# Performance work log

Hardware: AMD Instinct MI355X
Metric: run time of the kernel (lower is better)

Reference implementation:

```python
import jax, jax.numpy as jnp
import numpy as np

B, C, D = 4, 512, 1024
N = 8           # num_experts
DFF = 4096      # GEGLU inner dim; in-projection outputs 2*DFF


def setup_inputs() -> dict:
    key = jax.random.key(0)
    ks = jax.random.split(key, 7)
    hidden_states = jax.random.normal(ks[0], (B, C, D), dtype=jnp.float32)
    # Dispatch mask: one-hot expert assignment per token (top-1 routing).
    assign = jax.random.randint(ks[1], (B, C), 0, N)
    dispatch_mask = jax.nn.one_hot(assign, N, dtype=jnp.float32)        # [B,C,N]
    # Combine mask: same sparsity pattern, scaled by a router probability.
    probs = jax.random.uniform(ks[2], (B, C, 1), dtype=jnp.float32)
    combine_mask = dispatch_mask * probs                                 # [B,C,N]
    s_in = 1.0 / np.sqrt(D)
    s_out = 1.0 / np.sqrt(DFF)
    W_in = jax.random.normal(ks[3], (N, 2 * DFF, D), dtype=jnp.float32) * s_in
    b_in = jax.random.normal(ks[4], (N, 2 * DFF), dtype=jnp.float32) * 0.01
    W_out = jax.random.normal(ks[5], (N, D, DFF), dtype=jnp.float32) * s_out
    b_out = jax.random.normal(ks[6], (N, D), dtype=jnp.float32) * 0.01
    return {"hidden_states": hidden_states, "dispatch_mask": dispatch_mask,
            "combine_mask": combine_mask, "W_in": W_in, "b_in": b_in,
            "W_out": W_out, "b_out": b_out}


def reference(hidden_states, dispatch_mask, combine_mask, W_in, b_in, W_out, b_out):
    # Dispatch: [B,C,D] x [B,C,N] -> [N,B,C,D]
    h = jnp.einsum('bcd,bcn->nbcd', hidden_states, dispatch_mask)
    # Per-expert GEGLU FFN.
    h = jnp.einsum('nbcd,nfd->nbcf', h, W_in) + b_in[:, None, None, :]   # [N,B,C,2*DFF]
    x, gate = jnp.split(h, 2, axis=-1)
    h = x * jax.nn.gelu(gate, approximate=False)                          # torch F.gelu = exact erf
    h = jnp.einsum('nbcd,nfd->nbcf', h, W_out) + b_out[:, None, None, :]  # [N,B,C,D]
    # Combine: [N,B,C,D] x [B,C,N] -> [B,C,D]
    return jnp.einsum('nbcd,bcn->bcd', h, combine_mask)
```

## Files before the change

kernel.cpp:

```cpp
#include <hip/hip_runtime.h>
#include <math.h>

#define NTOK 2048
#define DDIM 1024
#define NEXP 8
#define DFF 4096
#define TWODFF 8192

typedef __attribute__((ext_vector_type(8))) short bf16x8;
typedef __attribute__((ext_vector_type(4))) float f32x4;

__device__ __forceinline__ short f2bf(float f) {
  unsigned u = __builtin_bit_cast(unsigned, f);
  u = (u + 0x7FFFu + ((u >> 16) & 1u)) >> 16;
  return (short)u;
}

__device__ __forceinline__ unsigned pk2(float a, float b) {
  unsigned r;
  asm("v_cvt_pk_bf16_f32 %0, %1, %2" : "=v"(r) : "v"(a), "v"(b));
  return r;
}

__device__ __forceinline__ void ldsbar() {
  asm volatile("s_waitcnt lgkmcnt(0)" ::: "memory");
  __builtin_amdgcn_s_barrier();
}

__global__ void route_k(const float* __restrict__ disp, const float* __restrict__ comb,
                        int* __restrict__ cnt, int* __restrict__ tokl,
                        float* __restrict__ scale) {
  __shared__ int lcnt[NEXP];
  const int tid = threadIdx.x;
  if (tid < NEXP) lcnt[tid] = 0;
  __syncthreads();
  for (int i = 0; i < 8; ++i) {
    const int t = i * 256 + tid;
    const float* row = disp + (size_t)t * NEXP;
    int e = 0;
#pragma unroll
    for (int n = 1; n < NEXP; ++n) e = (row[n] > row[e]) ? n : e;
    const float p = comb[(size_t)t * NEXP + e];
    const int slot = atomicAdd(&lcnt[e], 1);
    tokl[e * NTOK + slot] = t;
    scale[t] = p;
  }
  __syncthreads();
  if (tid < NEXP) cnt[tid] = lcnt[tid];
}

#define G1_LOAD(sa, sb, k0) do {                                              \
  _Pragma("unroll") for (int i_ = 0; i_ < 4; ++i_) {                          \
    sb[i_] = *(const float4*)(bP[i_] + (k0));                                 \
    sa[i_] = aP[i_] ? *(const float4*)(aP[i_] + (k0))                         \
                    : make_float4(0.f, 0.f, 0.f, 0.f);                        \
  } } while (0)

#define G1_STORE(sa, sb, buf) do {                                            \
  _Pragma("unroll") for (int i_ = 0; i_ < 4; ++i_) {                          \
    const int row_ = i_ * 32 + r0;                                            \
    const int off_ = row_ * 80 + (tid & 7) * 8;                               \
    uint2 va_, vb_;                                                           \
    va_.x = pk2(sa[i_].x, sa[i_].y); va_.y = pk2(sa[i_].z, sa[i_].w);         \
    vb_.x = pk2(sb[i_].x, sb[i_].y); vb_.y = pk2(sb[i_].z, sb[i_].w);         \
    *(uint2*)(Al[buf] + off_) = va_;                                          \
    *(uint2*)(Bl[buf] + off_) = vb_;                                          \
  } } while (0)

__global__ __launch_bounds__(256) void gemm1_k(
    const float* __restrict__ hid, const float* __restrict__ Win,
    const float* __restrict__ bin, const int* __restrict__ cnt,
    const int* __restrict__ tokl, short* __restrict__ act) {
  const int e = blockIdx.z;
  const int Me = cnt[e];
  const int m0 = blockIdx.y * 128;
  if (m0 >= Me) return;
  const int f0 = blockIdx.x * 64;

  __shared__ char Al[2][128 * 80];
  __shared__ char Bl[2][128 * 80];
  __shared__ int tokids[128];

  const int tid = threadIdx.x;
  if (tid < 128) {
    const int r = m0 + tid;
    tokids[tid] = (r < Me) ? tokl[e * NTOK + r] : -1;
  }
  __syncthreads();

  const int r0 = tid >> 3;
  const int c0 = (tid & 7) * 4;
  const float* aP[4];
  const float* bP[4];
#pragma unroll
  for (int i = 0; i < 4; ++i) {
    const int row = i * 32 + r0;
    const int tk = tokids[row];
    aP[i] = (tk >= 0) ? (hid + (size_t)tk * DDIM + c0) : nullptr;
    const int wr = (row < 64) ? (f0 + row) : (DFF + f0 + (row - 64));
    bP[i] = Win + (size_t)e * TWODFF * DDIM + (size_t)wr * DDIM + c0;
  }

  const int wid = tid >> 6, lane = tid & 63;
  const int wm = (wid >> 1) * 64;
  const int wf = (wid & 1) * 32;
  const int lr = lane & 15;
  const int kc = (lane >> 4) * 16;

  f32x4 accx[4][2], accg[4][2];
  const f32x4 zf = {0.f, 0.f, 0.f, 0.f};
#pragma unroll
  for (int a = 0; a < 4; ++a)
#pragma unroll
    for (int b = 0; b < 2; ++b) { accx[a][b] = zf; accg[a][b] = zf; }

  float4 sAa[4], sBa[4], sAb[4], sBb[4];
  G1_LOAD(sAa, sBa, 0);
  G1_STORE(sAa, sBa, 0);
  G1_LOAD(sAb, sBb, 32);
  ldsbar();

  for (int kt = 0; kt < 32; ++kt) {
    if (kt < 30) {
      if (kt & 1) G1_LOAD(sAb, sBb, (kt + 2) * 32);
      else        G1_LOAD(sAa, sBa, (kt + 2) * 32);
    }
    const char* Ab = Al[kt & 1];
    const char* Bb = Bl[kt & 1];
    bf16x8 a[4], bx[2], bg[2];
#pragma unroll
    for (int fm = 0; fm < 4; ++fm) {
      const int row = wm + fm * 16 + lr;
      a[fm] = *(const bf16x8*)(Ab + row * 80 + kc);
    }
#pragma unroll
    for (int ff = 0; ff < 2; ++ff) {
      const int rx = wf + ff * 16 + lr;
      bx[ff] = *(const bf16x8*)(Bb + rx * 80 + kc);
      bg[ff] = *(const bf16x8*)(Bb + (rx + 64) * 80 + kc);
    }
#pragma unroll
    for (int fm = 0; fm < 4; ++fm)
#pragma unroll
      for (int ff = 0; ff < 2; ++ff) {
        accx[fm][ff] = __builtin_amdgcn_mfma_f32_16x16x32_bf16(a[fm], bx[ff], accx[fm][ff], 0, 0, 0);
        accg[fm][ff] = __builtin_amdgcn_mfma_f32_16x16x32_bf16(a[fm], bg[ff], accg[fm][ff], 0, 0, 0);
      }
    if (kt < 31) {
      if (kt & 1) G1_STORE(sAa, sBa, (kt + 1) & 1);
      else        G1_STORE(sAb, sBb, (kt + 1) & 1);
    }
    ldsbar();
  }

  const int orb = (lane >> 4) * 4;
#pragma unroll
  for (int ff = 0; ff < 2; ++ff) {
    const int fcol = f0 + wf + ff * 16 + lr;
    const float bx_ = bin[e * TWODFF + fcol];
    const float bg_ = bin[e * TWODFF + DFF + fcol];
#pragma unroll
    for (int fm = 0; fm < 4; ++fm)
#pragma unroll
      for (int j = 0; j < 4; ++j) {
        const int row = wm + fm * 16 + orb + j;
        if (m0 + row < Me) {
          const float x = accx[fm][ff][j] + bx_;
          const float g = accg[fm][ff][j] + bg_;
          const float gl = 0.5f * g * (1.f + erff(g * 0.70710678118654752f));
          act[(size_t)tokids[row] * DFF + fcol] = f2bf(x * gl);
        }
      }
  }
}

__global__ __launch_bounds__(256) void gemm2_k(
    const short* __restrict__ act, const float* __restrict__ Wout,
    const float* __restrict__ bout, const int* __restrict__ cnt,
    const int* __restrict__ tokl, const float* __restrict__ scale,
    float* __restrict__ out) {
  const int e = blockIdx.z;
  const int Me = cnt[e];
  const int m0 = blockIdx.y * 128;
  if (m0 >= Me) return;
  const int n0 = blockIdx.x * 64;

  __shared__ short Al[2][128 * 64];
  __shared__ short Bl[2][64 * 64];
  __shared__ int tokids[128];
  __shared__ float pv[128];

  const int tid = threadIdx.x;
  if (tid < 128) {
    const int r = m0 + tid;
    const int tk = (r < Me) ? tokl[e * NTOK + r] : -1;
    tokids[tid] = tk;
    pv[tid] = (tk >= 0) ? scale[tk] : 0.f;
  }
  __syncthreads();

  const int ar0 = tid >> 3;
  const int ac0 = (tid & 7) * 8;
  const short* aP[4];
#pragma unroll
  for (int i = 0; i < 4; ++i) {
    const int row = i * 32 + ar0;
    const int tk = tokids[row];
    aP[i] = (tk >= 0) ? (act + (size_t)tk * DFF + ac0) : nullptr;
  }
  const int br0 = tid >> 4;
  const float* bP[4];
#pragma unroll
  for (int i = 0; i < 4; ++i) {
    const int row = i * 16 + br0;
    bP[i] = Wout + (size_t)e * DDIM * DFF + (size_t)(n0 + row) * DFF + (tid & 15) * 4;
  }

  bf16x8 aR[4];
  float4 bR[4];
  auto load_t = [&](int k0) {
#pragma unroll
    for (int i = 0; i < 4; ++i) bR[i] = *(const float4*)(bP[i] + k0);
    const bf16x8 z = {0, 0, 0, 0, 0, 0, 0, 0};
#pragma unroll
    for (int i = 0; i < 4; ++i) aR[i] = aP[i] ? *(const bf16x8*)(aP[i] + k0) : z;
  };
  auto store_t = [&](int buf) {
#pragma unroll
    for (int i = 0; i < 4; ++i) {
      const int row = i * 32 + ar0;
      const int ba = (row * 128 + (tid & 7) * 16) ^ ((row & 7) << 4);
      *(bf16x8*)((char*)Al[buf] + ba) = aR[i];
    }
#pragma unroll
    for (int i = 0; i < 4; ++i) {
      const int row = i * 16 + br0;
      const int bb = (row * 128 + (tid & 15) * 8) ^ ((row & 7) << 4);
      uint2 vb;
      vb.x = pk2(bR[i].x, bR[i].y); vb.y = pk2(bR[i].z, bR[i].w);
      *(uint2*)((char*)Bl[buf] + bb) = vb;
    }
  };

  const int wid = tid >> 6, lane = tid & 63;
  const int wm = (wid >> 1) * 64;
  const int wn = (wid & 1) * 32;
  const int lr = lane & 15;
  const int lkb = (lane >> 4) * 16;

  f32x4 acc[4][2];
  const f32x4 zf = {0.f, 0.f, 0.f, 0.f};
#pragma unroll
  for (int a = 0; a < 4; ++a) { acc[a][0] = zf; acc[a][1] = zf; }

  load_t(0);
  store_t(0);

  for (int kt = 0; kt < 64; ++kt) {
    if (kt < 63) load_t((kt + 1) * 64);
    __syncthreads();
    const char* Ab = (const char*)Al[kt & 1];
    const char* Bb = (const char*)Bl[kt & 1];
#pragma unroll
    for (int ks = 0; ks < 2; ++ks) {
      bf16x8 a[4], b[2];
      const int kb = ks * 64 + lkb;
#pragma unroll
      for (int fm = 0; fm < 4; ++fm) {
        const int row = wm + fm * 16 + lr;
        a[fm] = *(const bf16x8*)(Ab + ((row * 128 + kb) ^ ((row & 7) << 4)));
      }
#pragma unroll
      for (int ff = 0; ff < 2; ++ff) {
        const int rn = wn + ff * 16 + lr;
        b[ff] = *(const bf16x8*)(Bb + ((rn * 128 + kb) ^ ((rn & 7) << 4)));
      }
#pragma unroll
      for (int fm = 0; fm < 4; ++fm)
#pragma unroll
        for (int ff = 0; ff < 2; ++ff)
          acc[fm][ff] = __builtin_amdgcn_mfma_f32_16x16x32_bf16(a[fm], b[ff], acc[fm][ff], 0, 0, 0);
    }
    if (kt < 63) store_t((kt + 1) & 1);
  }

  const int orb = (lane >> 4) * 4;
#pragma unroll
  for (int ff = 0; ff < 2; ++ff) {
    const int ncol = n0 + wn + ff * 16 + lr;
    const float bo = bout[e * DDIM + ncol];
#pragma unroll
    for (int fm = 0; fm < 4; ++fm)
#pragma unroll
      for (int j = 0; j < 4; ++j) {
        const int row = wm + fm * 16 + orb + j;
        if (m0 + row < Me)
          out[(size_t)tokids[row] * DDIM + ncol] = pv[row] * (acc[fm][ff][j] + bo);
      }
  }
}

extern "C" void kernel_launch(void* const* d_in, const int* in_sizes, int n_in,
                              void* d_out, int out_size, void* d_ws, size_t ws_size,
                              hipStream_t stream) {
  const float* hid = (const float*)d_in[0];
  const float* disp = (const float*)d_in[1];
  const float* comb = (const float*)d_in[2];
  const float* Win = (const float*)d_in[3];
  const float* bin = (const float*)d_in[4];
  const float* Wout = (const float*)d_in[5];
  const float* bout = (const float*)d_in[6];
  float* out = (float*)d_out;

  char* ws = (char*)d_ws;
  int* cnt = (int*)(ws);
  int* tokl = (int*)(ws + 256);
  float* scale = (float*)(ws + 256 + NTOK * NEXP * 4);
  short* act = (short*)(ws + (1 << 17));

  route_k<<<1, 256, 0, stream>>>(disp, comb, cnt, tokl, scale);
  gemm1_k<<<dim3(DFF / 64, 4, NEXP), 256, 0, stream>>>(hid, Win, bin, cnt, tokl, act);
  gemm2_k<<<dim3(DDIM / 64, 4, NEXP), 256, 0, stream>>>(act, Wout, bout, cnt, tokl, scale, out);
}
```

Baseline: 247.8 us.

## Pre-convert hidden states to bf16, widen K tile with swizzled LDS in gemm1

A new kernel converts the hidden states to bf16 once, so gemm1 loads A tiles as bf16 and does not reconvert the same rows for every f-tile. gemm1 now uses a 64-wide K tile (16 iterations instead of 32) with an XOR-swizzled 128-byte LDS row layout in place of 80-byte padding. It also uses a flattened 1D grid with the expert index in the low bits, so work from different experts is interleaved. The aim is fewer barriers, less redundant conversion and fewer LDS bank conflicts, at the cost of an extra launch and more LDS per block, which may lower occupancy.

```diff
diff --git a/kernel.cpp b/kernel.cpp
--- a/kernel.cpp
+++ b/kernel.cpp
@@ -49,63 +49,84 @@
   if (tid < NEXP) cnt[tid] = lcnt[tid];
 }
 
-#define G1_LOAD(sa, sb, k0) do {                                              \
+__global__ __launch_bounds__(256) void cvt_k(const float* __restrict__ hid,
+                                             short* __restrict__ hidb) {
+  const int t = blockIdx.x * 256 + threadIdx.x;
+#pragma unroll
+  for (int i = 0; i < 16; ++i) {
+    const float4 v = ((const float4*)hid)[i * 32768 + t];
+    uint2 o;
+    o.x = pk2(v.x, v.y);
+    o.y = pk2(v.z, v.w);
+    ((uint2*)hidb)[i * 32768 + t] = o;
+  }
+}
+
+#define G1_LOAD(k0) do {                                                      \
+  _Pragma("unroll") for (int i_ = 0; i_ < 8; ++i_)                            \
+    sB[i_] = *(const float4*)(bP[i_] + (k0));                                 \
+  _Pragma("unroll") for (int i_ = 0; i_ < 4; ++i_)                            \
+    sA[i_] = aP[i_] ? *(const bf16x8*)(aP[i_] + (k0)) : zro;                  \
+  } while (0)
+
+#define G1_STORE(buf) do {                                                    \
   _Pragma("unroll") for (int i_ = 0; i_ < 4; ++i_) {                          \
-    sb[i_] = *(const float4*)(bP[i_] + (k0));                                 \
-    sa[i_] = aP[i_] ? *(const float4*)(aP[i_] + (k0))                         \
-                    : make_float4(0.f, 0.f, 0.f, 0.f);                        \
+    const int row_ = i_ * 32 + (tid >> 3);                                    \
+    const int ba_ = (row_ * 128 + (tid & 7) * 16) ^ ((row_ & 7) << 4);        \
+    *(bf16x8*)(Al[buf] + ba_) = sA[i_];                                       \
+  }                                                                           \
+  _Pragma("unroll") for (int i_ = 0; i_ < 8; ++i_) {                          \
+    const int row_ = i_ * 16 + (tid >> 4);                                    \
+    const int bb_ = (row_ * 128 + (tid & 15) * 8) ^ ((row_ & 7) << 4);        \
+    uint2 vb_;                                                                \
+    vb_.x = pk2(sB[i_].x, sB[i_].y); vb_.y = pk2(sB[i_].z, sB[i_].w);         \
+    *(uint2*)(Bl[buf] + bb_) = vb_;                                           \
   } } while (0)
 
-#define G1_STORE(sa, sb, buf) do {                                            \
-  _Pragma("unroll") for (int i_ = 0; i_ < 4; ++i_) {                          \
-    const int row_ = i_ * 32 + r0;                                            \
-    const int off_ = row_ * 80 + (tid & 7) * 8;                               \
-    uint2 va_, vb_;                                                           \
-    va_.x = pk2(sa[i_].x, sa[i_].y); va_.y = pk2(sa[i_].z, sa[i_].w);         \
-    vb_.x = pk2(sb[i_].x, sb[i_].y); vb_.y = pk2(sb[i_].z, sb[i_].w);         \
-    *(uint2*)(Al[buf] + off_) = va_;                                          \
-    *(uint2*)(Bl[buf] + off_) = vb_;                                          \
-  } } while (0)
-
 __global__ __launch_bounds__(256) void gemm1_k(
-    const float* __restrict__ hid, const float* __restrict__ Win,
+    const short* __restrict__ hidb, const float* __restrict__ Win,
     const float* __restrict__ bin, const int* __restrict__ cnt,
     const int* __restrict__ tokl, short* __restrict__ act) {
-  const int e = blockIdx.z;
+  const int bid = blockIdx.x;
+  const int e = bid & 7;
+  const int r = bid >> 3;
+  const int f0 = (r & 63) * 64;
+  const int m0 = (r >> 6) * 128;
   const int Me = cnt[e];
-  const int m0 = blockIdx.y * 128;
   if (m0 >= Me) return;
-  const int f0 = blockIdx.x * 64;
-
-  __shared__ char Al[2][128 * 80];
-  __shared__ char Bl[2][128 * 80];
+
+  __shared__ char Al[2][128 * 128];
+  __shared__ char Bl[2][128 * 128];
   __shared__ int tokids[128];
 
   const int tid = threadIdx.x;
   if (tid < 128) {
-    const int r = m0 + tid;
-    tokids[tid] = (r < Me) ? tokl[e * NTOK + r] : -1;
+    const int rr = m0 + tid;
+    tokids[tid] = (rr < Me) ? tokl[e * NTOK + rr] : -1;
   }
   __syncthreads();
 
-  const int r0 = tid >> 3;
-  const int c0 = (tid & 7) * 4;
-  const float* aP[4];
-  const float* bP[4];
+  const short* aP[4];
 #pragma unroll
   for (int i = 0; i < 4; ++i) {
-    const int row = i * 32 + r0;
+    const int row = i * 32 + (tid >> 3);
     const int tk = tokids[row];
-    aP[i] = (tk >= 0) ? (hid + (size_t)tk * DDIM + c0) : nullptr;
+    aP[i] = (tk >= 0) ? (hidb + (size_t)tk * DDIM + (tid & 7) * 8) : nullptr;
+  }
+  const float* bP[8];
+#pragma unroll
+  for (int i = 0; i < 8; ++i) {
+    const int row = i * 16 + (tid >> 4);
     const int wr = (row < 64) ? (f0 + row) : (DFF + f0 + (row - 64));
-    bP[i] = Win + (size_t)e * TWODFF * DDIM + (size_t)wr * DDIM + c0;
-  }
-
+    bP[i] = Win + (size_t)e * TWODFF * DDIM + (size_t)wr * DDIM + (tid & 15) * 4;
+  }
+
+  const bf16x8 zro = {0, 0, 0, 0, 0, 0, 0, 0};
   const int wid = tid >> 6, lane = tid & 63;
   const int wm = (wid >> 1) * 64;
   const int wf = (wid & 1) * 32;
   const int lr = lane & 15;
-  const int kc = (lane >> 4) * 16;
+  const int lkb = (lane >> 4) * 16;
 
   f32x4 accx[4][2], accg[4][2];
   const f32x4 zf = {0.f, 0.f, 0.f, 0.f};
@@ -114,43 +135,41 @@
 #pragma unroll
     for (int b = 0; b < 2; ++b) { accx[a][b] = zf; accg[a][b] = zf; }
 
-  float4 sAa[4], sBa[4], sAb[4], sBb[4];
-  G1_LOAD(sAa, sBa, 0);
-  G1_STORE(sAa, sBa, 0);
-  G1_LOAD(sAb, sBb, 32);
-  ldsbar();
-
-  for (int kt = 0; kt < 32; ++kt) {
-    if (kt < 30) {
-      if (kt & 1) G1_LOAD(sAb, sBb, (kt + 2) * 32);
-      else        G1_LOAD(sAa, sBa, (kt + 2) * 32);
-    }
+  bf16x8 sA[4];
+  float4 sB[8];
+  G1_LOAD(0);
+  G1_STORE(0);
+
+  for (int kt = 0; kt < 16; ++kt) {
+    ldsbar();
+    if (kt < 15) G1_LOAD((kt + 1) * 64);
     const char* Ab = Al[kt & 1];
     const char* Bb = Bl[kt & 1];
-    bf16x8 a[4], bx[2], bg[2];
-#pragma unroll
-    for (int fm = 0; fm < 4; ++fm) {
-      const int row = wm + fm * 16 + lr;
-      a[fm] = *(const bf16x8*)(Ab + row * 80 + kc);
+#pragma unroll
+    for (int ks = 0; ks < 2; ++ks) {
+      const int kb = ks * 64 + lkb;
+      bf16x8 a[4], bx[2], bg[2];
+#pragma unroll
+      for (int fm = 0; fm < 4; ++fm) {
+        const int row = wm + fm * 16 + lr;
+        a[fm] = *(const bf16x8*)(Ab + ((row * 128 + kb) ^ ((row & 7) << 4)));
+      }
+#pragma unroll
+      for (int ff = 0; ff < 2; ++ff) {
+        const int rx = wf + ff * 16 + lr;
+        bx[ff] = *(const bf16x8*)(Bb + ((rx * 128 + kb) ^ ((rx & 7) << 4)));
+        const int rg = rx + 64;
+        bg[ff] = *(const bf16x8*)(Bb + ((rg * 128 + kb) ^ ((rg & 7) << 4)));
+      }
+#pragma unroll
+      for (int fm = 0; fm < 4; ++fm)
+#pragma unroll
+        for (int ff = 0; ff < 2; ++ff) {
+          accx[fm][ff] = __builtin_amdgcn_mfma_f32_16x16x32_bf16(a[fm], bx[ff], accx[fm][ff], 0, 0, 0);
+          accg[fm][ff] = __builtin_amdgcn_mfma_f32_16x16x32_bf16(a[fm], bg[ff], accg[fm][ff], 0, 0, 0);
+        }
     }
-#pragma unroll
-    for (int ff = 0; ff < 2; ++ff) {
-      const int rx = wf + ff * 16 + lr;
-      bx[ff] = *(const bf16x8*)(Bb + rx * 80 + kc);
-      bg[ff] = *(const bf16x8*)(Bb + (rx + 64) * 80 + kc);
-    }
-#pragma unroll
-    for (int fm = 0; fm < 4; ++fm)
-#pragma unroll
-      for (int ff = 0; ff < 2; ++ff) {
-        accx[fm][ff] = __builtin_amdgcn_mfma_f32_16x16x32_bf16(a[fm], bx[ff], accx[fm][ff], 0, 0, 0);
-        accg[fm][ff] = __builtin_amdgcn_mfma_f32_16x16x32_bf16(a[fm], bg[ff], accg[fm][ff], 0, 0, 0);
-      }
-    if (kt < 31) {
-      if (kt & 1) G1_STORE(sAa, sBa, (kt + 1) & 1);
-      else        G1_STORE(sAb, sBb, (kt + 1) & 1);
-    }
-    ldsbar();
+    if (kt < 15) G1_STORE((kt + 1) & 1);
   }
 
   const int orb = (lane >> 4) * 4;
@@ -317,8 +336,10 @@
   int* tokl = (int*)(ws + 256);
   float* scale = (float*)(ws + 256 + NTOK * NEXP * 4);
   short* act = (short*)(ws + (1 << 17));
+  short* hidb = (short*)(ws + (1 << 17) + NTOK * DFF * 2);
 
   route_k<<<1, 256, 0, stream>>>(disp, comb, cnt, tokl, scale);
-  gemm1_k<<<dim3(DFF / 64, 4, NEXP), 256, 0, stream>>>(hid, Win, bin, cnt, tokl, act);
+  cvt_k<<<128, 256, 0, stream>>>(hid, hidb);
+  gemm1_k<<<2048, 256, 0, stream>>>(hidb, Win, bin, cnt, tokl, act);
   gemm2_k<<<dim3(DDIM / 64, 4, NEXP), 256, 0, stream>>>(act, Wout, bout, cnt, tokl, scale, out);
 }
```

Measured after the change: 248.2 us. No clear change (+0.2%).
